# Performance work log

Measured on AMD Instinct MI355X. Metric: run time of the kernel, lower is better.

## Reference

```python
import jax, jax.numpy as jnp
import numpy as np

K_HEADS = 8
D_HEAD = 64
D = K_HEADS * D_HEAD  # 512
B, TP, TQ, N = 8, 48, 48, 256


def setup_inputs() -> dict:
    key = jax.random.key(0)
    ks = jax.random.split(key, 13)
    s = 1.0 / np.sqrt(D)
    inp = {
        "X": jax.random.normal(ks[0], (B, TP, N, D), jnp.float32),
        "STE_P": jax.random.normal(ks[1], (B, TP, N, D), jnp.float32),
        "STE_Q": jax.random.normal(ks[2], (B, TQ, N, D), jnp.float32),
        "Wq": jax.random.uniform(ks[3], (D, D), jnp.float32, -s, s),
        "bq": jax.random.uniform(ks[4], (D,), jnp.float32, -s, s),
        "Wk": jax.random.uniform(ks[5], (D, D), jnp.float32, -s, s),
        "bk": jax.random.uniform(ks[6], (D,), jnp.float32, -s, s),
        "Wv": jax.random.uniform(ks[7], (D, D), jnp.float32, -s, s),
        "bv": jax.random.uniform(ks[8], (D,), jnp.float32, -s, s),
        "W1": jax.random.uniform(ks[9], (D, D), jnp.float32, -s, s),
        "b1": jax.random.uniform(ks[10], (D,), jnp.float32, -s, s),
        "W2": jax.random.uniform(ks[11], (D, D), jnp.float32, -s, s),
        "b2": jax.random.uniform(ks[12], (D,), jnp.float32, -s, s),
    }
    return inp


def reference(X, STE_P, STE_Q, Wq, bq, Wk, bk, Wv, bv, W1, b1, W2, b2):
    # ReLU-fused QKV projections
    q = jax.nn.relu(STE_Q @ Wq + bq)  # [B, Tq, N, D]
    k = jax.nn.relu(STE_P @ Wk + bk)  # [B, Tp, N, D]
    v = jax.nn.relu(X @ Wv + bv)      # [B, Tp, N, D]

    # split(last, d) + cat(dim 0) == introduce head axis h of size K
    b, tq, n, _ = q.shape
    tp = k.shape[1]
    q = q.reshape(b, tq, n, K_HEADS, D_HEAD)
    k = k.reshape(b, tp, n, K_HEADS, D_HEAD)
    v = v.reshape(b, tp, n, K_HEADS, D_HEAD)

    # attention over the TIME axis, per node and head: scores [b,h,n,tq,tp]
    scale = 1.0 / jnp.sqrt(jnp.asarray(D_HEAD, q.dtype))
    attn = jnp.einsum('bqnhd,bpnhd->bhnqp', q, k) * scale
    attn = jax.nn.softmax(attn, axis=-1)
    out = jnp.einsum('bhnqp,bpnhd->bqnhd', attn, v).reshape(b, tq, n, D)

    out = jax.nn.relu(out @ W1 + b1) @ W2 + b2
    return out
```

## Files before the change

### kernel.cpp

```cpp
#include <hip/hip_runtime.h>

typedef _Float16 f16;
typedef _Float16 f16x4 __attribute__((ext_vector_type(4)));
typedef _Float16 f16x8 __attribute__((ext_vector_type(8)));
typedef float f32x4 __attribute__((ext_vector_type(4)));

typedef const __attribute__((address_space(1))) unsigned int guint;
typedef __attribute__((address_space(3))) unsigned int luint;
__device__ __forceinline__ void gl_lds16(const void* g, void* l) {
    __builtin_amdgcn_global_load_lds((guint*)g, (luint*)l, 16, 0, 0);
}

__global__ __launch_bounds__(256) void wconv(const float* w0, const float* w1, const float* w2,
                                             const float* w3, const float* w4, f16* dst) {
    const float* src;
    switch (blockIdx.z) { case 0: src = w0; break; case 1: src = w1; break;
                          case 2: src = w2; break; case 3: src = w3; break; default: src = w4; }
    __shared__ float tile[32][33];
    int k0 = blockIdx.x * 32, n0 = blockIdx.y * 32;
    int t = threadIdx.x;
    int r = t >> 3, c4 = (t & 7) * 4;
    float4 v = *(const float4*)(src + (k0 + r) * 512 + n0 + c4);
    tile[r][c4 + 0] = v.x; tile[r][c4 + 1] = v.y; tile[r][c4 + 2] = v.z; tile[r][c4 + 3] = v.w;
    __syncthreads();
    f16x4 o;
    o[0] = (f16)tile[c4 + 0][r]; o[1] = (f16)tile[c4 + 1][r];
    o[2] = (f16)tile[c4 + 2][r]; o[3] = (f16)tile[c4 + 3][r];
    *(f16x4*)(dst + (size_t)blockIdx.z * 262144 + (n0 + r) * 512 + k0 + c4) = o;
}

template <bool A16, bool RELU, bool O16>
__global__ __launch_bounds__(256) void gemm_lds(const void* __restrict__ Ap,
                                                const f16* __restrict__ Bt,
                                                const float* __restrict__ bias,
                                                void* __restrict__ Cp) {
    constexpr int ASZ = A16 ? 8192 : 16384;
    constexpr int BSZ = 8192;
    constexpr int BUF = ASZ + BSZ;
    __shared__ __align__(16) char smem[2 * BUF];

    const int cpx = gridDim.x >> 3;
    const int orig = blockIdx.x;
    const int wgid = (orig & 7) * cpx + (orig >> 3);
    const int by = wgid & 3;
    const int bx = wgid >> 2;
    const int r0 = bx * 128, c0 = by * 128;

    const int t = threadIdx.x;
    const int j = t & 63, w = t >> 6;
    const int lr = j & 15, lq = j >> 4;
    const int wr = (w >> 1) * 64, wc = (w & 1) * 64;

    const int ldsT = w * 1024 + j * 16;
    const char* aSrc;
    if (A16) {
        int rt = w * 16 + (j >> 2);
        int sb = (j & 3) ^ ((j >> 2) & 3);
        aSrc = (const char*)Ap + ((size_t)(r0 + rt) * 512 + sb * 8) * 2;
    } else {
        int rt = w * 8 + (j >> 3);
        int sb = (j & 7) ^ (j >> 3);
        aSrc = (const char*)Ap + ((size_t)(r0 + rt) * 512 + sb * 4) * 4;
    }
    const char* bSrc;
    {
        int rt = w * 16 + (j >> 2);
        int sb = (j & 3) ^ ((j >> 2) & 3);
        bSrc = (const char*)Bt + ((size_t)(c0 + rt) * 512 + sb * 8) * 2;
    }
    const int aBytesPerK = A16 ? 64 : 128;

    int aoffL[4], aoffH[4], boff[4];
#pragma unroll
    for (int m = 0; m < 4; m++) {
        int row = wr + m * 16 + lr;
        if (A16) {
            aoffL[m] = row * 64 + ((lq ^ (row & 3)) << 4);
        } else {
            int s = row & 7;
            aoffL[m] = row * 128 + (((2 * lq) ^ s) << 4);
            aoffH[m] = row * 128 + (((2 * lq + 1) ^ s) << 4);
        }
    }
#pragma unroll
    for (int nb = 0; nb < 4; nb++) {
        int row = wc + nb * 16 + lr;
        boff[nb] = ASZ + row * 64 + ((lq ^ (row & 3)) << 4);
    }

    f32x4 acc[4][4] = {};

#define STAGE(tk, buf)                                                        \
    do {                                                                      \
        const char* as_ = aSrc + (size_t)(tk) * aBytesPerK;                   \
        char* al_ = smem + (buf) * BUF + ldsT;                                \
        gl_lds16(as_, al_);                                                   \
        gl_lds16(as_ + 65536, al_ + 4096);                                    \
        if (!A16) {                                                           \
            gl_lds16(as_ + 131072, al_ + 8192);                               \
            gl_lds16(as_ + 196608, al_ + 12288);                              \
        }                                                                     \
        const char* bs_ = bSrc + (size_t)(tk) * 64;                           \
        char* bl_ = smem + (buf) * BUF + ASZ + ldsT;                          \
        gl_lds16(bs_, bl_);                                                   \
        gl_lds16(bs_ + 65536, bl_ + 4096);                                    \
    } while (0)

    STAGE(0, 0);
    __syncthreads();

    int cur = 0;
#pragma unroll 1
    for (int tk = 0; tk < 16; ++tk) {
        if (tk < 15) STAGE(tk + 1, cur ^ 1);
        const char* sb = smem + cur * BUF;
        f16x8 av[4], bv[4];
#pragma unroll
        for (int m = 0; m < 4; m++) {
            if (A16) {
                av[m] = *(const f16x8*)(sb + aoffL[m]);
            } else {
                float4 x0 = *(const float4*)(sb + aoffL[m]);
                float4 x1 = *(const float4*)(sb + aoffH[m]);
                f16x8 h;
                h[0] = (f16)x0.x; h[1] = (f16)x0.y; h[2] = (f16)x0.z; h[3] = (f16)x0.w;
                h[4] = (f16)x1.x; h[5] = (f16)x1.y; h[6] = (f16)x1.z; h[7] = (f16)x1.w;
                av[m] = h;
            }
        }
#pragma unroll
        for (int nb = 0; nb < 4; nb++) bv[nb] = *(const f16x8*)(sb + boff[nb]);
#pragma unroll
        for (int m = 0; m < 4; m++)
#pragma unroll
            for (int nb = 0; nb < 4; nb++)
                acc[m][nb] = __builtin_amdgcn_mfma_f32_16x16x32_f16(av[m], bv[nb], acc[m][nb], 0, 0, 0);
        __syncthreads();
        cur ^= 1;
    }
#undef STAGE

#pragma unroll
    for (int nb = 0; nb < 4; nb++) {
        int col = c0 + wc + nb * 16 + lr;
        float b = bias[col];
#pragma unroll
        for (int m = 0; m < 4; m++) {
#pragma unroll
            for (int r = 0; r < 4; r++) {
                float v = acc[m][nb][r] + b;
                if (RELU) v = fmaxf(v, 0.0f);
                size_t row = (size_t)(r0 + wr + m * 16 + lq * 4 + r);
                if (O16) ((f16*)Cp)[row * 512 + col] = (f16)v;
                else     ((float*)Cp)[row * 512 + col] = v;
            }
        }
    }
}

__global__ __launch_bounds__(64) void attn_kernel(const f16* __restrict__ q,
                                                  const f16* __restrict__ k,
                                                  const f16* __restrict__ v,
                                                  f16* __restrict__ out) {
    const int h = blockIdx.x, n = blockIdx.y, b = blockIdx.z;
    __shared__ f16 sQ[48 * 72];
    __shared__ f16 sK[48 * 72];
    __shared__ f16 sP[48 * 72];
    __shared__ f16 sVt[64 * 72];
    const int l = threadIdx.x, lr = l & 15, lq = l >> 4;
    const size_t rowstride = 256 * 512;
    const size_t base = ((size_t)(b * 48) * 256 + n) * 512 + h * 64;

    const int pr = l >> 3, pc = (l & 7) * 8;
#pragma unroll
    for (int pass = 0; pass < 6; pass++) {
        int row = pass * 8 + pr;
        size_t g = base + (size_t)row * rowstride + pc;
        f16x8 qv = *(const f16x8*)(q + g);
        f16x8 kv = *(const f16x8*)(k + g);
        f16x8 vv = *(const f16x8*)(v + g);
        *(f16x8*)&sQ[row * 72 + pc] = qv;
        *(f16x8*)&sK[row * 72 + pc] = kv;
#pragma unroll
        for (int j = 0; j < 8; j++) sVt[(pc + j) * 72 + row] = vv[j];
    }
    {
        f16x8 z = {};
        *(f16x8*)&sVt[l * 72 + 48] = z;
        *(f16x8*)&sVt[l * 72 + 56] = z;
        if (l < 48) { *(f16x8*)&sP[l * 72 + 48] = z; *(f16x8*)&sP[l * 72 + 56] = z; }
    }
    __syncthreads();

    f32x4 s[3][3] = {};
#pragma unroll
    for (int ks = 0; ks < 2; ks++) {
        f16x8 aq[3], bk[3];
#pragma unroll
        for (int m = 0; m < 3; m++)  aq[m] = *(const f16x8*)&sQ[(m * 16 + lr) * 72 + ks * 32 + lq * 8];
#pragma unroll
        for (int nb = 0; nb < 3; nb++) bk[nb] = *(const f16x8*)&sK[(nb * 16 + lr) * 72 + ks * 32 + lq * 8];
#pragma unroll
        for (int m = 0; m < 3; m++)
#pragma unroll
            for (int nb = 0; nb < 3; nb++)
                s[m][nb] = __builtin_amdgcn_mfma_f32_16x16x32_f16(aq[m], bk[nb], s[m][nb], 0, 0, 0);
    }

#pragma unroll
    for (int m = 0; m < 3; m++) {
#pragma unroll
        for (int r = 0; r < 4; r++) {
            float a0 = s[m][0][r] * 0.125f, a1 = s[m][1][r] * 0.125f, a2 = s[m][2][r] * 0.125f;
            float mx = fmaxf(a0, fmaxf(a1, a2));
#pragma unroll
            for (int d = 1; d < 16; d <<= 1) mx = fmaxf(mx, __shfl_xor(mx, d));
            float e0 = __expf(a0 - mx), e1 = __expf(a1 - mx), e2 = __expf(a2 - mx);
            float sm = e0 + e1 + e2;
#pragma unroll
            for (int d = 1; d < 16; d <<= 1) sm += __shfl_xor(sm, d);
            float inv = 1.0f / sm;
            int row = m * 16 + lq * 4 + r;
            sP[row * 72 + 0  + lr] = (f16)(e0 * inv);
            sP[row * 72 + 16 + lr] = (f16)(e1 * inv);
            sP[row * 72 + 32 + lr] = (f16)(e2 * inv);
        }
    }
    __syncthreads();

    f32x4 o[3][4] = {};
#pragma unroll
    for (int ks = 0; ks < 2; ks++) {
        f16x8 ap[3], bvv[4];
#pragma unroll
        for (int m = 0; m < 3; m++)  ap[m] = *(const f16x8*)&sP[(m * 16 + lr) * 72 + ks * 32 + lq * 8];
#pragma unroll
        for (int nb = 0; nb < 4; nb++) bvv[nb] = *(const f16x8*)&sVt[(nb * 16 + lr) * 72 + ks * 32 + lq * 8];
#pragma unroll
        for (int m = 0; m < 3; m++)
#pragma unroll
            for (int nb = 0; nb < 4; nb++)
                o[m][nb] = __builtin_amdgcn_mfma_f32_16x16x32_f16(ap[m], bvv[nb], o[m][nb], 0, 0, 0);
    }

#pragma unroll
    for (int m = 0; m < 3; m++)
#pragma unroll
        for (int nb = 0; nb < 4; nb++)
#pragma unroll
            for (int r = 0; r < 4; r++) {
                int row = m * 16 + lq * 4 + r;
                out[base + (size_t)row * rowstride + nb * 16 + lr] = (f16)o[m][nb][r];
            }
}

extern "C" void kernel_launch(void* const* d_in, const int* in_sizes, int n_in,
                              void* d_out, int out_size, void* d_ws, size_t ws_size,
                              hipStream_t stream) {
    const float* X    = (const float*)d_in[0];
    const float* STEP = (const float*)d_in[1];
    const float* STEQ = (const float*)d_in[2];
    const float* Wq   = (const float*)d_in[3];
    const float* bq   = (const float*)d_in[4];
    const float* Wk   = (const float*)d_in[5];
    const float* bk   = (const float*)d_in[6];
    const float* Wv   = (const float*)d_in[7];
    const float* bv   = (const float*)d_in[8];
    const float* W1   = (const float*)d_in[9];
    const float* b1   = (const float*)d_in[10];
    const float* W2   = (const float*)d_in[11];
    const float* b2   = (const float*)d_in[12];
    float* out = (float*)d_out;

    const size_t MROWS = 98304;
    f16* ws  = (f16*)d_ws;
    f16* Wqt = ws;
    f16* Wkt = ws + 262144;
    f16* Wvt = ws + 524288;
    f16* W1t = ws + 786432;
    f16* W2t = ws + 1048576;
    f16* qb  = ws + 1310720;
    f16* kb  = qb + MROWS * 512;
    f16* vb  = kb + MROWS * 512;
    f16* attn = qb;
    f16* hb   = kb;

    wconv<<<dim3(16, 16, 5), 256, 0, stream>>>(Wq, Wk, Wv, W1, W2, ws);

    gemm_lds<false, true, true><<<3072, 256, 0, stream>>>(STEQ, Wqt, bq, qb);
    gemm_lds<false, true, true><<<3072, 256, 0, stream>>>(STEP, Wkt, bk, kb);
    gemm_lds<false, true, true><<<3072, 256, 0, stream>>>(X,    Wvt, bv, vb);

    attn_kernel<<<dim3(8, 256, 8), 64, 0, stream>>>(qb, kb, vb, attn);

    gemm_lds<true, true,  true ><<<3072, 256, 0, stream>>>(attn, W1t, b1, hb);
    gemm_lds<true, false, false><<<3072, 256, 0, stream>>>(hb,   W2t, b2, out);
}
```

Before: 634.3 us.

## Convert fp32 A tiles to fp16 in registers before LDS store in GEMM

For fp32 A inputs, the GEMM now loads A through registers, converts to fp16 with packed round-toward-zero conversions, and writes fp16 to LDS, instead of staging fp32 directly to LDS via global_load_lds and converting on every LDS read. This halves the LDS footprint and LDS read traffic for the A tile and changes the swizzle pattern. The register-staged path loses the asynchronous direct-to-LDS load, so load latency is hidden by software pipelining across the compute step. Round-toward-zero also slightly changes rounding compared with the default conversion.

```diff
diff --git a/kernel.cpp b/kernel.cpp
--- a/kernel.cpp
+++ b/kernel.cpp
@@ -1,6 +1,7 @@
 #include <hip/hip_runtime.h>
 
 typedef _Float16 f16;
+typedef __fp16 hf2 __attribute__((ext_vector_type(2)));
 typedef _Float16 f16x4 __attribute__((ext_vector_type(4)));
 typedef _Float16 f16x8 __attribute__((ext_vector_type(8)));
 typedef float f32x4 __attribute__((ext_vector_type(4)));
@@ -34,9 +35,8 @@
                                                 const f16* __restrict__ Bt,
                                                 const float* __restrict__ bias,
                                                 void* __restrict__ Cp) {
-    constexpr int ASZ = A16 ? 8192 : 16384;
-    constexpr int BSZ = 8192;
-    constexpr int BUF = ASZ + BSZ;
+    constexpr int ASZ = 8192;
+    constexpr int BUF = 16384;
     __shared__ __align__(16) char smem[2 * BUF];
 
     const int cpx = gridDim.x >> 3;
@@ -52,93 +52,120 @@
     const int wr = (w >> 1) * 64, wc = (w & 1) * 64;
 
     const int ldsT = w * 1024 + j * 16;
-    const char* aSrc;
-    if (A16) {
-        int rt = w * 16 + (j >> 2);
-        int sb = (j & 3) ^ ((j >> 2) & 3);
-        aSrc = (const char*)Ap + ((size_t)(r0 + rt) * 512 + sb * 8) * 2;
-    } else {
-        int rt = w * 8 + (j >> 3);
-        int sb = (j & 7) ^ (j >> 3);
-        aSrc = (const char*)Ap + ((size_t)(r0 + rt) * 512 + sb * 4) * 4;
-    }
-    const char* bSrc;
-    {
-        int rt = w * 16 + (j >> 2);
-        int sb = (j & 3) ^ ((j >> 2) & 3);
-        bSrc = (const char*)Bt + ((size_t)(c0 + rt) * 512 + sb * 8) * 2;
-    }
-    const int aBytesPerK = A16 ? 64 : 128;
-
-    int aoffL[4], aoffH[4], boff[4];
+    const int sb = (j & 3) ^ ((j >> 3) & 3);
+    const char* bSrc = (const char*)Bt + ((size_t)(c0 + w * 16 + (j >> 2)) * 512 + sb * 8) * 2;
+    const char* aSrc16 = (const char*)Ap + ((size_t)(r0 + w * 16 + (j >> 2)) * 512 + sb * 8) * 2;
+    const char* aSrc32 = (const char*)Ap + ((size_t)(r0 + (t >> 1)) * 512 + (t & 1) * 16) * 4;
+    const int awRow = t >> 1;
+    const int awS = (awRow >> 1) & 3;
+    const int awc = (t & 1) * 2;
+    const int aw0 = awRow * 64 + ((awc ^ awS) << 4);
+    const int aw1 = awRow * 64 + (((awc + 1) ^ awS) << 4);
+
+    int aoff[4], boff[4];
 #pragma unroll
     for (int m = 0; m < 4; m++) {
         int row = wr + m * 16 + lr;
-        if (A16) {
-            aoffL[m] = row * 64 + ((lq ^ (row & 3)) << 4);
-        } else {
-            int s = row & 7;
-            aoffL[m] = row * 128 + (((2 * lq) ^ s) << 4);
-            aoffH[m] = row * 128 + (((2 * lq + 1) ^ s) << 4);
-        }
+        aoff[m] = row * 64 + ((lq ^ ((row >> 1) & 3)) << 4);
     }
 #pragma unroll
     for (int nb = 0; nb < 4; nb++) {
         int row = wc + nb * 16 + lr;
-        boff[nb] = ASZ + row * 64 + ((lq ^ (row & 3)) << 4);
+        boff[nb] = ASZ + row * 64 + ((lq ^ ((row >> 1) & 3)) << 4);
     }
 
     f32x4 acc[4][4] = {};
 
-#define STAGE(tk, buf)                                                        \
-    do {                                                                      \
-        const char* as_ = aSrc + (size_t)(tk) * aBytesPerK;                   \
-        char* al_ = smem + (buf) * BUF + ldsT;                                \
-        gl_lds16(as_, al_);                                                   \
-        gl_lds16(as_ + 65536, al_ + 4096);                                    \
-        if (!A16) {                                                           \
-            gl_lds16(as_ + 131072, al_ + 8192);                               \
-            gl_lds16(as_ + 196608, al_ + 12288);                              \
-        }                                                                     \
-        const char* bs_ = bSrc + (size_t)(tk) * 64;                           \
-        char* bl_ = smem + (buf) * BUF + ASZ + ldsT;                          \
-        gl_lds16(bs_, bl_);                                                   \
-        gl_lds16(bs_ + 65536, bl_ + 4096);                                    \
-    } while (0)
-
-    STAGE(0, 0);
-    __syncthreads();
-
-    int cur = 0;
+#define STAGE_B(tk, buf)                                      \
+    do {                                                      \
+        const char* bs_ = bSrc + (size_t)(tk) * 64;           \
+        char* bl_ = smem + (buf) * BUF + ASZ + ldsT;          \
+        gl_lds16(bs_, bl_);                                   \
+        gl_lds16(bs_ + 65536, bl_ + 4096);                    \
+    } while (0)
+#define STAGE_A16(tk, buf)                                    \
+    do {                                                      \
+        const char* as_ = aSrc16 + (size_t)(tk) * 64;         \
+        char* al_ = smem + (buf) * BUF + ldsT;                \
+        gl_lds16(as_, al_);                                   \
+        gl_lds16(as_ + 65536, al_ + 4096);                    \
+    } while (0)
+#define LOAD_A32(tk, ar)                                      \
+    do {                                                      \
+        const char* p_ = aSrc32 + (size_t)(tk) * 128;         \
+        ar[0] = *(const float4*)(p_);                         \
+        ar[1] = *(const float4*)(p_ + 16);                    \
+        ar[2] = *(const float4*)(p_ + 32);                    \
+        ar[3] = *(const float4*)(p_ + 48);                    \
+    } while (0)
+#define WRITE_A32(ar, buf)                                    \
+    do {                                                      \
+        hf2 p0_ = __builtin_amdgcn_cvt_pkrtz(ar[0].x, ar[0].y); \
+        hf2 p1_ = __builtin_amdgcn_cvt_pkrtz(ar[0].z, ar[0].w); \
+        hf2 p2_ = __builtin_amdgcn_cvt_pkrtz(ar[1].x, ar[1].y); \
+        hf2 p3_ = __builtin_amdgcn_cvt_pkrtz(ar[1].z, ar[1].w); \
+        hf2 p4_ = __builtin_amdgcn_cvt_pkrtz(ar[2].x, ar[2].y); \
+        hf2 p5_ = __builtin_amdgcn_cvt_pkrtz(ar[2].z, ar[2].w); \
+        hf2 p6_ = __builtin_amdgcn_cvt_pkrtz(ar[3].x, ar[3].y); \
+        hf2 p7_ = __builtin_amdgcn_cvt_pkrtz(ar[3].z, ar[3].w); \
+        f16x8 h0_, h1_;                                       \
+        h0_[0] = (f16)p0_[0]; h0_[1] = (f16)p0_[1]; h0_[2] = (f16)p1_[0]; h0_[3] = (f16)p1_[1]; \
+        h0_[4] = (f16)p2_[0]; h0_[5] = (f16)p2_[1]; h0_[6] = (f16)p3_[0]; h0_[7] = (f16)p3_[1]; \
+        h1_[0] = (f16)p4_[0]; h1_[1] = (f16)p4_[1]; h1_[2] = (f16)p5_[0]; h1_[3] = (f16)p5_[1]; \
+        h1_[4] = (f16)p6_[0]; h1_[5] = (f16)p6_[1]; h1_[6] = (f16)p7_[0]; h1_[7] = (f16)p7_[1]; \
+        char* base_ = smem + (buf) * BUF;                     \
+        *(f16x8*)(base_ + aw0) = h0_;                         \
+        *(f16x8*)(base_ + aw1) = h1_;                         \
+    } while (0)
+#define COMPUTE(buf)                                          \
+    do {                                                      \
+        const char* sb_ = smem + (buf) * BUF;                 \
+        f16x8 av[4], bv[4];                                   \
+        _Pragma("unroll")                                     \
+        for (int m = 0; m < 4; m++) av[m] = *(const f16x8*)(sb_ + aoff[m]); \
+        _Pragma("unroll")                                     \
+        for (int nb = 0; nb < 4; nb++) bv[nb] = *(const f16x8*)(sb_ + boff[nb]); \
+        _Pragma("unroll")                                     \
+        for (int m = 0; m < 4; m++)                           \
+            _Pragma("unroll")                                 \
+            for (int nb = 0; nb < 4; nb++)                    \
+                acc[m][nb] = __builtin_amdgcn_mfma_f32_16x16x32_f16(av[m], bv[nb], acc[m][nb], 0, 0, 0); \
+    } while (0)
+
+    if (A16) {
+        STAGE_A16(0, 0);
+        STAGE_B(0, 0);
+        __syncthreads();
+        int cur = 0;
 #pragma unroll 1
-    for (int tk = 0; tk < 16; ++tk) {
-        if (tk < 15) STAGE(tk + 1, cur ^ 1);
-        const char* sb = smem + cur * BUF;
-        f16x8 av[4], bv[4];
-#pragma unroll
-        for (int m = 0; m < 4; m++) {
-            if (A16) {
-                av[m] = *(const f16x8*)(sb + aoffL[m]);
-            } else {
-                float4 x0 = *(const float4*)(sb + aoffL[m]);
-                float4 x1 = *(const float4*)(sb + aoffH[m]);
-                f16x8 h;
-                h[0] = (f16)x0.x; h[1] = (f16)x0.y; h[2] = (f16)x0.z; h[3] = (f16)x0.w;
-                h[4] = (f16)x1.x; h[5] = (f16)x1.y; h[6] = (f16)x1.z; h[7] = (f16)x1.w;
-                av[m] = h;
-            }
+        for (int tk = 0; tk < 16; ++tk) {
+            if (tk < 15) { STAGE_A16(tk + 1, cur ^ 1); STAGE_B(tk + 1, cur ^ 1); }
+            COMPUTE(cur);
+            __syncthreads();
+            cur ^= 1;
         }
-#pragma unroll
-        for (int nb = 0; nb < 4; nb++) bv[nb] = *(const f16x8*)(sb + boff[nb]);
-#pragma unroll
-        for (int m = 0; m < 4; m++)
-#pragma unroll
-            for (int nb = 0; nb < 4; nb++)
-                acc[m][nb] = __builtin_amdgcn_mfma_f32_16x16x32_f16(av[m], bv[nb], acc[m][nb], 0, 0, 0);
+    } else {
+        float4 ar[4];
+        LOAD_A32(0, ar);
+        STAGE_B(0, 0);
+        WRITE_A32(ar, 0);
         __syncthreads();
-        cur ^= 1;
-    }
-#undef STAGE
+        int cur = 0;
+#pragma unroll 1
+        for (int tk = 0; tk < 16; ++tk) {
+            float4 an[4];
+            if (tk < 15) { LOAD_A32(tk + 1, an); STAGE_B(tk + 1, cur ^ 1); }
+            COMPUTE(cur);
+            if (tk < 15) WRITE_A32(an, cur ^ 1);
+            __syncthreads();
+            cur ^= 1;
+        }
+    }
+#undef STAGE_B
+#undef STAGE_A16
+#undef LOAD_A32
+#undef WRITE_A32
+#undef COMPUTE
 
 #pragma unroll
     for (int nb = 0; nb < 4; nb++) {
```

Result: slower. 713.9 us (+12.6%).

## Deepen GEMM LDS pipeline to four buffers with vmcnt waits and single barrier

Applied to the files above, without the earlier changes.

Replaces the double-buffered GEMM loop with a 4-stage ring of LDS buffers. Three K-tiles are prefetched ahead, and each step waits on a partial vmcnt with a raw barrier instead of a full __syncthreads, so global->LDS loads overlap compute more deeply. It also switches fp32->fp16 conversion to packed cvt_pkrtz (round-toward-zero instead of round-to-nearest), raises wave priority around the MFMA block, and changes the load/swizzle mapping. The cost is double the LDS per block, which may reduce occupancy, plus slightly different rounding.

```diff
diff --git a/kernel.cpp b/kernel.cpp
--- a/kernel.cpp
+++ b/kernel.cpp
@@ -1,6 +1,7 @@
 #include <hip/hip_runtime.h>
 
 typedef _Float16 f16;
+typedef __fp16 hf2 __attribute__((ext_vector_type(2)));
 typedef _Float16 f16x4 __attribute__((ext_vector_type(4)));
 typedef _Float16 f16x8 __attribute__((ext_vector_type(8)));
 typedef float f32x4 __attribute__((ext_vector_type(4)));
@@ -10,6 +11,16 @@
 __device__ __forceinline__ void gl_lds16(const void* g, void* l) {
     __builtin_amdgcn_global_load_lds((guint*)g, (luint*)l, 16, 0, 0);
 }
+
+template <int N>
+__device__ __forceinline__ void vmwait() {
+    if constexpr (N == 12)      asm volatile("s_waitcnt vmcnt(12)" ::: "memory");
+    else if constexpr (N == 8)  asm volatile("s_waitcnt vmcnt(8)" ::: "memory");
+    else if constexpr (N == 6)  asm volatile("s_waitcnt vmcnt(6)" ::: "memory");
+    else if constexpr (N == 4)  asm volatile("s_waitcnt vmcnt(4)" ::: "memory");
+    else                        asm volatile("s_waitcnt vmcnt(0)" ::: "memory");
+}
+__device__ __forceinline__ void barrier_raw() { __builtin_amdgcn_s_barrier(); __builtin_amdgcn_sched_barrier(0); }
 
 __global__ __launch_bounds__(256) void wconv(const float* w0, const float* w1, const float* w2,
                                              const float* w3, const float* w4, f16* dst) {
@@ -30,14 +41,14 @@
 }
 
 template <bool A16, bool RELU, bool O16>
-__global__ __launch_bounds__(256) void gemm_lds(const void* __restrict__ Ap,
-                                                const f16* __restrict__ Bt,
-                                                const float* __restrict__ bias,
-                                                void* __restrict__ Cp) {
+__global__ __launch_bounds__(256) void gemm_p4(const void* __restrict__ Ap,
+                                               const f16* __restrict__ Bt,
+                                               const float* __restrict__ bias,
+                                               void* __restrict__ Cp) {
     constexpr int ASZ = A16 ? 8192 : 16384;
     constexpr int BSZ = 8192;
     constexpr int BUF = ASZ + BSZ;
-    __shared__ __align__(16) char smem[2 * BUF];
+    __shared__ __align__(16) char smem[4 * BUF];
 
     const int cpx = gridDim.x >> 3;
     const int orig = blockIdx.x;
@@ -51,31 +62,17 @@
     const int lr = j & 15, lq = j >> 4;
     const int wr = (w >> 1) * 64, wc = (w & 1) * 64;
 
-    const int ldsT = w * 1024 + j * 16;
     const char* aSrc;
-    if (A16) {
-        int rt = w * 16 + (j >> 2);
-        int sb = (j & 3) ^ ((j >> 2) & 3);
-        aSrc = (const char*)Ap + ((size_t)(r0 + rt) * 512 + sb * 8) * 2;
-    } else {
-        int rt = w * 8 + (j >> 3);
-        int sb = (j & 7) ^ (j >> 3);
-        aSrc = (const char*)Ap + ((size_t)(r0 + rt) * 512 + sb * 4) * 4;
-    }
-    const char* bSrc;
-    {
-        int rt = w * 16 + (j >> 2);
-        int sb = (j & 3) ^ ((j >> 2) & 3);
-        bSrc = (const char*)Bt + ((size_t)(c0 + rt) * 512 + sb * 8) * 2;
-    }
-    const int aBytesPerK = A16 ? 64 : 128;
+    if (A16) aSrc = (const char*)Ap + ((size_t)(r0 + (t >> 2)) * 512 + ((t & 3) ^ ((t >> 3) & 3)) * 8) * 2;
+    else     aSrc = (const char*)Ap + ((size_t)(r0 + (t >> 3)) * 512 + ((t & 7) ^ ((t >> 3) & 7)) * 4) * 4;
+    const char* bSrc = (const char*)Bt + ((size_t)(c0 + (t >> 2)) * 512 + ((t & 3) ^ ((t >> 3) & 3)) * 8) * 2;
 
     int aoffL[4], aoffH[4], boff[4];
 #pragma unroll
     for (int m = 0; m < 4; m++) {
         int row = wr + m * 16 + lr;
         if (A16) {
-            aoffL[m] = row * 64 + ((lq ^ (row & 3)) << 4);
+            aoffL[m] = row * 64 + ((lq ^ ((row >> 1) & 3)) << 4);
         } else {
             int s = row & 7;
             aoffL[m] = row * 128 + (((2 * lq) ^ s) << 4);
@@ -85,60 +82,72 @@
 #pragma unroll
     for (int nb = 0; nb < 4; nb++) {
         int row = wc + nb * 16 + lr;
-        boff[nb] = ASZ + row * 64 + ((lq ^ (row & 3)) << 4);
+        boff[nb] = ASZ + row * 64 + ((lq ^ ((row >> 1) & 3)) << 4);
     }
 
     f32x4 acc[4][4] = {};
 
-#define STAGE(tk, buf)                                                        \
-    do {                                                                      \
-        const char* as_ = aSrc + (size_t)(tk) * aBytesPerK;                   \
-        char* al_ = smem + (buf) * BUF + ldsT;                                \
-        gl_lds16(as_, al_);                                                   \
-        gl_lds16(as_ + 65536, al_ + 4096);                                    \
-        if (!A16) {                                                           \
-            gl_lds16(as_ + 131072, al_ + 8192);                               \
-            gl_lds16(as_ + 196608, al_ + 12288);                              \
-        }                                                                     \
-        const char* bs_ = bSrc + (size_t)(tk) * 64;                           \
-        char* bl_ = smem + (buf) * BUF + ASZ + ldsT;                          \
-        gl_lds16(bs_, bl_);                                                   \
-        gl_lds16(bs_ + 65536, bl_ + 4096);                                    \
-    } while (0)
-
-    STAGE(0, 0);
-    __syncthreads();
-
-    int cur = 0;
-#pragma unroll 1
-    for (int tk = 0; tk < 16; ++tk) {
-        if (tk < 15) STAGE(tk + 1, cur ^ 1);
-        const char* sb = smem + cur * BUF;
+    auto stage = [&](int tk, int buf) {
+        const char* as_ = aSrc + (size_t)tk * (A16 ? 64 : 128);
+        char* al_ = smem + buf * BUF + t * 16;
+        gl_lds16(as_, al_);
+        gl_lds16(as_ + 65536, al_ + 4096);
+        if (!A16) {
+            gl_lds16(as_ + 131072, al_ + 8192);
+            gl_lds16(as_ + 196608, al_ + 12288);
+        }
+        const char* bs_ = bSrc + (size_t)tk * 64;
+        char* bl_ = smem + buf * BUF + ASZ + t * 16;
+        gl_lds16(bs_, bl_);
+        gl_lds16(bs_ + 65536, bl_ + 4096);
+    };
+
+    auto compute = [&](int buf) {
+        const char* sb_ = smem + buf * BUF;
         f16x8 av[4], bv[4];
 #pragma unroll
         for (int m = 0; m < 4; m++) {
             if (A16) {
-                av[m] = *(const f16x8*)(sb + aoffL[m]);
+                av[m] = *(const f16x8*)(sb_ + aoffL[m]);
             } else {
-                float4 x0 = *(const float4*)(sb + aoffL[m]);
-                float4 x1 = *(const float4*)(sb + aoffH[m]);
+                float4 x0 = *(const float4*)(sb_ + aoffL[m]);
+                float4 x1 = *(const float4*)(sb_ + aoffH[m]);
+                hf2 p0 = __builtin_amdgcn_cvt_pkrtz(x0.x, x0.y);
+                hf2 p1 = __builtin_amdgcn_cvt_pkrtz(x0.z, x0.w);
+                hf2 p2 = __builtin_amdgcn_cvt_pkrtz(x1.x, x1.y);
+                hf2 p3 = __builtin_amdgcn_cvt_pkrtz(x1.z, x1.w);
                 f16x8 h;
-                h[0] = (f16)x0.x; h[1] = (f16)x0.y; h[2] = (f16)x0.z; h[3] = (f16)x0.w;
-                h[4] = (f16)x1.x; h[5] = (f16)x1.y; h[6] = (f16)x1.z; h[7] = (f16)x1.w;
+                h[0] = (f16)p0[0]; h[1] = (f16)p0[1]; h[2] = (f16)p1[0]; h[3] = (f16)p1[1];
+                h[4] = (f16)p2[0]; h[5] = (f16)p2[1]; h[6] = (f16)p3[0]; h[7] = (f16)p3[1];
                 av[m] = h;
             }
         }
 #pragma unroll
-        for (int nb = 0; nb < 4; nb++) bv[nb] = *(const f16x8*)(sb + boff[nb]);
+        for (int nb = 0; nb < 4; nb++) bv[nb] = *(const f16x8*)(sb_ + boff[nb]);
+        __builtin_amdgcn_s_setprio(1);
 #pragma unroll
         for (int m = 0; m < 4; m++)
 #pragma unroll
             for (int nb = 0; nb < 4; nb++)
                 acc[m][nb] = __builtin_amdgcn_mfma_f32_16x16x32_f16(av[m], bv[nb], acc[m][nb], 0, 0, 0);
-        __syncthreads();
-        cur ^= 1;
-    }
-#undef STAGE
+        __builtin_amdgcn_s_setprio(0);
+    };
+
+    constexpr int STEADY = A16 ? 8 : 12;
+    constexpr int TAIL1  = A16 ? 4 : 6;
+
+    stage(0, 0); stage(1, 1); stage(2, 2);
+
+#pragma unroll 1
+    for (int tk = 0; tk < 13; ++tk) {
+        vmwait<STEADY>();
+        barrier_raw();
+        stage(tk + 3, (tk + 3) & 3);
+        compute(tk & 3);
+    }
+    vmwait<STEADY>(); barrier_raw(); compute(1);
+    vmwait<TAIL1>();  barrier_raw(); compute(2);
+    vmwait<0>();      barrier_raw(); compute(3);
 
 #pragma unroll
     for (int nb = 0; nb < 4; nb++) {
@@ -287,12 +296,12 @@
 
     wconv<<<dim3(16, 16, 5), 256, 0, stream>>>(Wq, Wk, Wv, W1, W2, ws);
 
-    gemm_lds<false, true, true><<<3072, 256, 0, stream>>>(STEQ, Wqt, bq, qb);
-    gemm_lds<false, true, true><<<3072, 256, 0, stream>>>(STEP, Wkt, bk, kb);
-    gemm_lds<false, true, true><<<3072, 256, 0, stream>>>(X,    Wvt, bv, vb);
+    gemm_p4<false, true, true><<<3072, 256, 0, stream>>>(STEQ, Wqt, bq, qb);
+    gemm_p4<false, true, true><<<3072, 256, 0, stream>>>(STEP, Wkt, bk, kb);
+    gemm_p4<false, true, true><<<3072, 256, 0, stream>>>(X,    Wvt, bv, vb);
 
     attn_kernel<<<dim3(8, 256, 8), 64, 0, stream>>>(qb, kb, vb, attn);
 
-    gemm_lds<true, true,  true ><<<3072, 256, 0, stream>>>(attn, W1t, b1, hb);
-    gemm_lds<true, false, false><<<3072, 256, 0, stream>>>(hb,   W2t, b2, out);
-}
+    gemm_p4<true, true,  true ><<<3072, 256, 0, stream>>>(attn, W1t, b1, hb);
+    gemm_p4<true, false, false><<<3072, 256, 0, stream>>>(hb,   W2t, b2, out);
+}
```

New measurement: 936.9 us. 47.7% more time.

## Use 256x128 GEMM tiles with 8 waves per block and packed f16 conversion

Applied to the files above, without the earlier changes.

The GEMM kernel now runs 512 threads (8 waves) per block over 256-row by 128-column output tiles, halving the grid. Each B tile loaded into LDS is shared by twice as many rows, which cuts B traffic per output element, and the simpler load mapping means every thread issues a single 16-byte async load per chunk. The LDS swizzle pattern is changed to match the new layout. The fp32-to-fp16 conversion of A now uses packed round-toward-zero conversions, which is cheaper but rounds differently. LDS per block doubles, to 80 KB for the fp32-A variant, which may reduce how many blocks fit on a CU.

```diff
diff --git a/kernel.cpp b/kernel.cpp
--- a/kernel.cpp
+++ b/kernel.cpp
@@ -1,6 +1,7 @@
 #include <hip/hip_runtime.h>
 
 typedef _Float16 f16;
+typedef __fp16 hf2 __attribute__((ext_vector_type(2)));
 typedef _Float16 f16x4 __attribute__((ext_vector_type(4)));
 typedef _Float16 f16x8 __attribute__((ext_vector_type(8)));
 typedef float f32x4 __attribute__((ext_vector_type(4)));
@@ -30,11 +31,11 @@
 }
 
 template <bool A16, bool RELU, bool O16>
-__global__ __launch_bounds__(256) void gemm_lds(const void* __restrict__ Ap,
-                                                const f16* __restrict__ Bt,
-                                                const float* __restrict__ bias,
-                                                void* __restrict__ Cp) {
-    constexpr int ASZ = A16 ? 8192 : 16384;
+__global__ __launch_bounds__(512) void gemm_w8(const void* __restrict__ Ap,
+                                               const f16* __restrict__ Bt,
+                                               const float* __restrict__ bias,
+                                               void* __restrict__ Cp) {
+    constexpr int ASZ = A16 ? 16384 : 32768;
     constexpr int BSZ = 8192;
     constexpr int BUF = ASZ + BSZ;
     __shared__ __align__(16) char smem[2 * BUF];
@@ -44,38 +45,24 @@
     const int wgid = (orig & 7) * cpx + (orig >> 3);
     const int by = wgid & 3;
     const int bx = wgid >> 2;
-    const int r0 = bx * 128, c0 = by * 128;
+    const int r0 = bx * 256, c0 = by * 128;
 
     const int t = threadIdx.x;
     const int j = t & 63, w = t >> 6;
     const int lr = j & 15, lq = j >> 4;
     const int wr = (w >> 1) * 64, wc = (w & 1) * 64;
 
-    const int ldsT = w * 1024 + j * 16;
     const char* aSrc;
-    if (A16) {
-        int rt = w * 16 + (j >> 2);
-        int sb = (j & 3) ^ ((j >> 2) & 3);
-        aSrc = (const char*)Ap + ((size_t)(r0 + rt) * 512 + sb * 8) * 2;
-    } else {
-        int rt = w * 8 + (j >> 3);
-        int sb = (j & 7) ^ (j >> 3);
-        aSrc = (const char*)Ap + ((size_t)(r0 + rt) * 512 + sb * 4) * 4;
-    }
-    const char* bSrc;
-    {
-        int rt = w * 16 + (j >> 2);
-        int sb = (j & 3) ^ ((j >> 2) & 3);
-        bSrc = (const char*)Bt + ((size_t)(c0 + rt) * 512 + sb * 8) * 2;
-    }
-    const int aBytesPerK = A16 ? 64 : 128;
+    if (A16) aSrc = (const char*)Ap + ((size_t)(r0 + (t >> 2)) * 512 + ((t & 3) ^ ((t >> 3) & 3)) * 8) * 2;
+    else     aSrc = (const char*)Ap + ((size_t)(r0 + (t >> 3)) * 512 + ((t & 7) ^ ((t >> 3) & 7)) * 4) * 4;
+    const char* bSrc = (const char*)Bt + ((size_t)(c0 + (t >> 2)) * 512 + ((t & 3) ^ ((t >> 3) & 3)) * 8) * 2;
 
     int aoffL[4], aoffH[4], boff[4];
 #pragma unroll
     for (int m = 0; m < 4; m++) {
         int row = wr + m * 16 + lr;
         if (A16) {
-            aoffL[m] = row * 64 + ((lq ^ (row & 3)) << 4);
+            aoffL[m] = row * 64 + ((lq ^ ((row >> 1) & 3)) << 4);
         } else {
             int s = row & 7;
             aoffL[m] = row * 128 + (((2 * lq) ^ s) << 4);
@@ -85,60 +72,71 @@
 #pragma unroll
     for (int nb = 0; nb < 4; nb++) {
         int row = wc + nb * 16 + lr;
-        boff[nb] = ASZ + row * 64 + ((lq ^ (row & 3)) << 4);
+        boff[nb] = ASZ + row * 64 + ((lq ^ ((row >> 1) & 3)) << 4);
     }
 
     f32x4 acc[4][4] = {};
 
-#define STAGE(tk, buf)                                                        \
-    do {                                                                      \
-        const char* as_ = aSrc + (size_t)(tk) * aBytesPerK;                   \
-        char* al_ = smem + (buf) * BUF + ldsT;                                \
-        gl_lds16(as_, al_);                                                   \
-        gl_lds16(as_ + 65536, al_ + 4096);                                    \
-        if (!A16) {                                                           \
-            gl_lds16(as_ + 131072, al_ + 8192);                               \
-            gl_lds16(as_ + 196608, al_ + 12288);                              \
-        }                                                                     \
-        const char* bs_ = bSrc + (size_t)(tk) * 64;                           \
-        char* bl_ = smem + (buf) * BUF + ASZ + ldsT;                          \
-        gl_lds16(bs_, bl_);                                                   \
-        gl_lds16(bs_ + 65536, bl_ + 4096);                                    \
+#define STAGE(tk, buf)                                                     \
+    do {                                                                   \
+        char* al_ = smem + (buf) * BUF + t * 16;                           \
+        if (A16) {                                                         \
+            const char* as_ = aSrc + (size_t)(tk) * 64;                    \
+            gl_lds16(as_, al_);                                            \
+            gl_lds16(as_ + 131072, al_ + 8192);                            \
+        } else {                                                           \
+            const char* as_ = aSrc + (size_t)(tk) * 128;                   \
+            gl_lds16(as_, al_);                                            \
+            gl_lds16(as_ + 131072, al_ + 8192);                            \
+            gl_lds16(as_ + 262144, al_ + 16384);                           \
+            gl_lds16(as_ + 393216, al_ + 24576);                           \
+        }                                                                  \
+        const char* bs_ = bSrc + (size_t)(tk) * 64;                        \
+        gl_lds16(bs_, smem + (buf) * BUF + ASZ + t * 16);                  \
     } while (0)
 
+#define COMPUTE(buf)                                                       \
+    do {                                                                   \
+        const char* sb_ = smem + (buf) * BUF;                              \
+        f16x8 av[4], bv[4];                                                \
+        _Pragma("unroll")                                                  \
+        for (int m = 0; m < 4; m++) {                                      \
+            if (A16) {                                                     \
+                av[m] = *(const f16x8*)(sb_ + aoffL[m]);                   \
+            } else {                                                       \
+                float4 x0 = *(const float4*)(sb_ + aoffL[m]);              \
+                float4 x1 = *(const float4*)(sb_ + aoffH[m]);              \
+                hf2 p0 = __builtin_amdgcn_cvt_pkrtz(x0.x, x0.y);           \
+                hf2 p1 = __builtin_amdgcn_cvt_pkrtz(x0.z, x0.w);           \
+                hf2 p2 = __builtin_amdgcn_cvt_pkrtz(x1.x, x1.y);           \
+                hf2 p3 = __builtin_amdgcn_cvt_pkrtz(x1.z, x1.w);           \
+                f16x8 h;                                                   \
+                h[0] = (f16)p0[0]; h[1] = (f16)p0[1]; h[2] = (f16)p1[0]; h[3] = (f16)p1[1]; \
+                h[4] = (f16)p2[0]; h[5] = (f16)p2[1]; h[6] = (f16)p3[0]; h[7] = (f16)p3[1]; \
+                av[m] = h;                                                 \
+            }                                                              \
+        }                                                                  \
+        _Pragma("unroll")                                                  \
+        for (int nb = 0; nb < 4; nb++) bv[nb] = *(const f16x8*)(sb_ + boff[nb]); \
+        _Pragma("unroll")                                                  \
+        for (int m = 0; m < 4; m++)                                        \
+            _Pragma("unroll")                                              \
+            for (int nb = 0; nb < 4; nb++)                                 \
+                acc[m][nb] = __builtin_amdgcn_mfma_f32_16x16x32_f16(av[m], bv[nb], acc[m][nb], 0, 0, 0); \
+    } while (0)
+
     STAGE(0, 0);
     __syncthreads();
-
     int cur = 0;
 #pragma unroll 1
     for (int tk = 0; tk < 16; ++tk) {
         if (tk < 15) STAGE(tk + 1, cur ^ 1);
-        const char* sb = smem + cur * BUF;
-        f16x8 av[4], bv[4];
-#pragma unroll
-        for (int m = 0; m < 4; m++) {
-            if (A16) {
-                av[m] = *(const f16x8*)(sb + aoffL[m]);
-            } else {
-                float4 x0 = *(const float4*)(sb + aoffL[m]);
-                float4 x1 = *(const float4*)(sb + aoffH[m]);
-                f16x8 h;
-                h[0] = (f16)x0.x; h[1] = (f16)x0.y; h[2] = (f16)x0.z; h[3] = (f16)x0.w;
-                h[4] = (f16)x1.x; h[5] = (f16)x1.y; h[6] = (f16)x1.z; h[7] = (f16)x1.w;
-                av[m] = h;
-            }
-        }
-#pragma unroll
-        for (int nb = 0; nb < 4; nb++) bv[nb] = *(const f16x8*)(sb + boff[nb]);
-#pragma unroll
-        for (int m = 0; m < 4; m++)
-#pragma unroll
-            for (int nb = 0; nb < 4; nb++)
-                acc[m][nb] = __builtin_amdgcn_mfma_f32_16x16x32_f16(av[m], bv[nb], acc[m][nb], 0, 0, 0);
+        COMPUTE(cur);
         __syncthreads();
         cur ^= 1;
     }
 #undef STAGE
+#undef COMPUTE
 
 #pragma unroll
     for (int nb = 0; nb < 4; nb++) {
@@ -287,12 +285,12 @@
 
     wconv<<<dim3(16, 16, 5), 256, 0, stream>>>(Wq, Wk, Wv, W1, W2, ws);
 
-    gemm_lds<false, true, true><<<3072, 256, 0, stream>>>(STEQ, Wqt, bq, qb);
-    gemm_lds<false, true, true><<<3072, 256, 0, stream>>>(STEP, Wkt, bk, kb);
-    gemm_lds<false, true, true><<<3072, 256, 0, stream>>>(X,    Wvt, bv, vb);
+    gemm_w8<false, true, true><<<1536, 512, 0, stream>>>(STEQ, Wqt, bq, qb);
+    gemm_w8<false, true, true><<<1536, 512, 0, stream>>>(STEP, Wkt, bk, kb);
+    gemm_w8<false, true, true><<<1536, 512, 0, stream>>>(X,    Wvt, bv, vb);
 
     attn_kernel<<<dim3(8, 256, 8), 64, 0, stream>>>(qb, kb, vb, attn);
 
-    gemm_lds<true, true,  true ><<<3072, 256, 0, stream>>>(attn, W1t, b1, hb);
-    gemm_lds<true, false, false><<<3072, 256, 0, stream>>>(hb,   W2t, b2, out);
-}
+    gemm_w8<true, true,  true ><<<1536, 512, 0, stream>>>(attn, W1t, b1, hb);
+    gemm_w8<true, false, false><<<1536, 512, 0, stream>>>(hb,   W2t, b2, out);
+}
```

Result: no change. 628.4 us (-0.9%).
